# Kernel tuning notes

Measured on AMD Instinct MI355X. Metric: run time of the kernel, lower is better.

The kernel has to match this reference:

```python
import jax, jax.numpy as jnp
import numpy as np

B, N, C, H, D = 4, 2048, 1024, 16, 64
EPS = 1e-6

def setup_inputs() -> dict:
    key = jax.random.key(0)
    k1, k2, k3 = jax.random.split(key, 3)
    hidden_states = jax.random.normal(k1, (B, N, C), dtype=jnp.float32)
    qkv_w = jax.random.normal(k2, (3 * C, C), dtype=jnp.float32) * (C ** -0.5)
    out_w = jax.random.normal(k3, (C, C), dtype=jnp.float32) * (C ** -0.5)
    norm_q_w = jnp.ones((D,), dtype=jnp.float32)
    norm_k_w = jnp.ones((D,), dtype=jnp.float32)
    # RoPE tables: standard theta=10000 frequencies, rotate-half convention
    inv_freq = 1.0 / (10000.0 ** (jnp.arange(0, D, 2, dtype=jnp.float32) / D))
    pos = jnp.arange(N, dtype=jnp.float32)
    angles = pos[:, None] * inv_freq[None, :]              # [N, D/2]
    angles = jnp.concatenate([angles, angles], axis=-1)    # [N, D]
    cos = jnp.cos(angles)
    sin = jnp.sin(angles)
    return {"hidden_states": hidden_states, "cos": cos, "sin": sin,
            "qkv_w": qkv_w, "out_w": out_w,
            "norm_q_w": norm_q_w, "norm_k_w": norm_k_w}

def _rms_norm(x, w):
    # RMSNorm over last dim (head_dim)
    var = jnp.mean(jnp.square(x), axis=-1, keepdims=True)
    return x * jax.lax.rsqrt(var + EPS) * w

def _rotate_half(x):
    x1, x2 = jnp.split(x, 2, axis=-1)
    return jnp.concatenate([-x2, x1], axis=-1)

def reference(hidden_states, cos, sin, qkv_w, out_w, norm_q_w, norm_k_w):
    # fused QKV projection: [B,N,C] -> [B,N,3,H,D]
    qkv = jnp.einsum('bnc,oc->bno', hidden_states, qkv_w).reshape(B, N, 3, H, D)
    q, k, v = qkv[:, :, 0], qkv[:, :, 1], qkv[:, :, 2]   # each [B,N,H,D]
    q = _rms_norm(q, norm_q_w)
    k = _rms_norm(k, norm_k_w)
    # RoPE, broadcast cos/sin [N,D] -> [1,N,1,D]
    c = cos[None, :, None, :]
    s = sin[None, :, None, :]
    q = q * c + _rotate_half(q) * s
    k = k * c + _rotate_half(k) * s
    # SDPA: softmax(q k^T / sqrt(D)) v, no mask
    scale = D ** -0.5
    scores = jnp.einsum('bqhd,bkhd->bhqk', q, k) * scale   # [B,H,N,N]
    probs = jax.nn.softmax(scores, axis=-1)
    attn = jnp.einsum('bhqk,bkhd->bqhd', probs, v).reshape(B, N, C)
    return jnp.einsum('bnc,oc->bno', attn, out_w)
```

## Files before the change

### kernel.cpp

```cpp
#include <hip/hip_runtime.h>
#include <hip/hip_bf16.h>

typedef short bf16x8 __attribute__((ext_vector_type(8)));
typedef float f32x4 __attribute__((ext_vector_type(4)));
typedef float f32x16 __attribute__((ext_vector_type(16)));
typedef __hip_bfloat16 bf16;
typedef unsigned int uint;

static constexpr int Bn = 4, Nn = 2048, Cn = 1024, Hn = 16, Dn = 64;
static constexpr float kEps = 1e-6f;
static constexpr float kQScale = 0.125f * 1.44269504088896340f;

#define GLOAD_LDS16(gp, lp)                                                        \
  __builtin_amdgcn_global_load_lds(                                                \
      (const __attribute__((address_space(1))) unsigned int*)(gp),                 \
      (__attribute__((address_space(3))) unsigned int*)(lp), 16, 0, 0)

__device__ __forceinline__ float exp2_raw(float x) {
  float r;
  asm("v_exp_f32 %0, %1" : "=v"(r) : "v"(x));
  return r;
}

__global__ __launch_bounds__(256) void cvt_kernel(const float* __restrict__ in,
                                                  bf16* __restrict__ out, int n4) {
  int i = blockIdx.x * 256 + threadIdx.x;
  if (i >= n4) return;
  const float4 v = reinterpret_cast<const float4*>(in)[i];
  bf16 t[4];
  t[0] = __float2bfloat16(v.x); t[1] = __float2bfloat16(v.y);
  t[2] = __float2bfloat16(v.z); t[3] = __float2bfloat16(v.w);
  reinterpret_cast<uint2*>(out)[i] = *reinterpret_cast<const uint2*>(t);
}

template <int EPI>
__global__ __launch_bounds__(256) void gemm_bt(
    const bf16* __restrict__ A, const bf16* __restrict__ Bw,
    float* __restrict__ Cf, bf16* __restrict__ q_raw, bf16* __restrict__ k_raw,
    bf16* __restrict__ v_buf, const float* __restrict__ cosb,
    const float* __restrict__ sinb, const float* __restrict__ nqw,
    const float* __restrict__ nkw, int N, int K) {
  __shared__ __align__(16) bf16 As[128 * 64];
  __shared__ __align__(16) bf16 Bs[128 * 64];
  const int tid = threadIdx.x;
  const int lane = tid & 63, w = tid >> 6;
  const int wr = w >> 1, wc = w & 1;
  const int l15 = lane & 15, l4 = lane >> 4;
  const int m0 = blockIdx.y * 128, n0 = blockIdx.x * 128;
  f32x4 acc[4][4] = {};

  const int sr = tid >> 3, sc = (tid & 7) * 8;
  const bf16* const Ap = A + (size_t)(m0 + sr) * K + sc;
  const bf16* const Bp = Bw + (size_t)(n0 + sr) * K + sc;
  char* const asd = (char*)As + tid * 16;
  char* const bsd = (char*)Bs + tid * 16;

  for (int k0 = 0; k0 < K; k0 += 64) {
    __syncthreads();
#pragma unroll
    for (int c = 0; c < 4; ++c) {
      GLOAD_LDS16(Ap + (size_t)(c * 32) * K + k0, asd + c * 4096);
      GLOAD_LDS16(Bp + (size_t)(c * 32) * K + k0, bsd + c * 4096);
    }
    __syncthreads();
#pragma unroll
    for (int kc = 0; kc < 2; ++kc) {
      bf16x8 af[4], bfr[4];
#pragma unroll
      for (int mi = 0; mi < 4; ++mi)
        af[mi] = *reinterpret_cast<const bf16x8*>(
            (const char*)As + (wr * 64 + mi * 16 + l15) * 128 + kc * 64 + l4 * 16);
#pragma unroll
      for (int ni = 0; ni < 4; ++ni)
        bfr[ni] = *reinterpret_cast<const bf16x8*>(
            (const char*)Bs + (wc * 64 + ni * 16 + l15) * 128 + kc * 64 + l4 * 16);
#pragma unroll
      for (int mi = 0; mi < 4; ++mi)
#pragma unroll
        for (int ni = 0; ni < 4; ++ni)
          acc[mi][ni] =
              __builtin_amdgcn_mfma_f32_16x16x32_bf16(af[mi], bfr[ni], acc[mi][ni], 0, 0, 0);
    }
  }

  if (EPI == 1) {
#pragma unroll
    for (int mi = 0; mi < 4; ++mi)
#pragma unroll
      for (int ni = 0; ni < 4; ++ni)
#pragma unroll
        for (int r = 0; r < 4; ++r) {
          const int row = m0 + wr * 64 + mi * 16 + l4 * 4 + r;
          const int col = n0 + wc * 64 + ni * 16 + l15;
          Cf[(size_t)row * N + col] = acc[mi][ni][r];
        }
    return;
  }

  const int colbase = n0 + wc * 64;
  const int which = colbase >> 10;
  const int hh = (colbase >> 6) & 15;
  if (which == 2) {
#pragma unroll
    for (int mi = 0; mi < 4; ++mi)
#pragma unroll
      for (int r = 0; r < 4; ++r) {
        const int row = m0 + wr * 64 + mi * 16 + l4 * 4 + r;
        const int b = row >> 11, n = row & (Nn - 1);
#pragma unroll
        for (int ni = 0; ni < 4; ++ni) {
          const int d = ni * 16 + l15;
          const size_t idx = (((size_t)b * Hn + hh) * Nn + n) * Dn + d;
          v_buf[idx] = __float2bfloat16(acc[mi][ni][r]);
        }
      }
    return;
  }
  const float* const wgt = which ? nkw : nqw;
  bf16* const dst = which ? k_raw : q_raw;
  float wv4[4];
#pragma unroll
  for (int ni = 0; ni < 4; ++ni) wv4[ni] = wgt[ni * 16 + l15];
#pragma unroll
  for (int mi = 0; mi < 4; ++mi)
#pragma unroll
    for (int r = 0; r < 4; ++r) {
      const int row = m0 + wr * 64 + mi * 16 + l4 * 4 + r;
      const int b = row >> 11, n = row & (Nn - 1);
      float x0 = acc[mi][0][r], x1 = acc[mi][1][r], x2 = acc[mi][2][r], x3 = acc[mi][3][r];
      float ss = x0 * x0 + x1 * x1 + x2 * x2 + x3 * x3;
      ss += __shfl_xor(ss, 1);
      ss += __shfl_xor(ss, 2);
      ss += __shfl_xor(ss, 4);
      ss += __shfl_xor(ss, 8);
      const float rinv = rsqrtf(ss * (1.f / Dn) + kEps);
      float nx[4] = {x0 * rinv * wv4[0], x1 * rinv * wv4[1], x2 * rinv * wv4[2],
                     x3 * rinv * wv4[3]};
#pragma unroll
      for (int ni = 0; ni < 4; ++ni) {
        const int d = ni * 16 + l15;
        const float c = cosb[n * Dn + d], s = sinb[n * Dn + d];
        const float sgn = (ni < 2) ? -1.f : 1.f;
        float val = nx[ni] * c + sgn * nx[ni ^ 2] * s;
        if (which == 0) val *= kQScale;
        const size_t idx = (((size_t)b * Hn + hh) * Nn + n) * Dn + d;
        dst[idx] = __float2bfloat16(val);
      }
    }
}

__global__ __launch_bounds__(256, 3) void flash_attn(
    const bf16* __restrict__ Qb, const bf16* __restrict__ Kb,
    const bf16* __restrict__ Vb, bf16* __restrict__ Ob) {
  __shared__ __align__(16) char KsB[2][32 * 128];
  __shared__ __align__(16) char VtB[2][64 * 64];
  const int bh = blockIdx.y;
  const int q0 = blockIdx.x * 128;
  const int tid = threadIdx.x, lane = tid & 63, w = tid >> 6;
  const int l31 = lane & 31, hi = lane >> 5;
  const bf16* Qp = Qb + (size_t)bh * Nn * Dn;
  const bf16* Kp = Kb + (size_t)bh * Nn * Dn;
  const bf16* Vp = Vb + (size_t)bh * Nn * Dn;

  const int qrow = q0 + w * 32 + l31;
  bf16x8 qf[4];
#pragma unroll
  for (int dm = 0; dm < 4; ++dm)
    qf[dm] = *reinterpret_cast<const bf16x8*>(&Qp[(size_t)qrow * Dn + dm * 16 + hi * 8]);

  f32x16 Ot0 = {}, Ot1 = {};
  float m_r = -1e30f, l_r = 0.f;

  const int skk = tid >> 3, sd0 = (tid & 7) * 8;
  const int srcKe = (((sd0 * 2) ^ ((skk & 7) << 4)) >> 1);

  auto stage_v = [&](char* Vn, const uint4& a) {
    const uint wa[4] = {a.x, a.y, a.z, a.w};
#pragma unroll
    for (int j = 0; j < 8; ++j) {
      const int d = sd0 + j;
      const int xs = (((d >> 1) ^ (d >> 3)) & 3) << 4;
      const unsigned short va = (j & 1) ? (unsigned short)(wa[j >> 1] >> 16)
                                        : (unsigned short)(wa[j >> 1] & 0xffff);
      *reinterpret_cast<unsigned short*>(Vn + d * 64 + ((skk * 2) ^ xs)) = va;
    }
  };

  GLOAD_LDS16(Kp + (size_t)skk * Dn + srcKe, KsB[0] + tid * 16);
  {
    uint4 cv = *reinterpret_cast<const uint4*>(&Vp[(size_t)skk * Dn + sd0]);
    stage_v(VtB[0], cv);
  }
  uint4 nv = *reinterpret_cast<const uint4*>(&Vp[(size_t)(32 + skk) * Dn + sd0]);
  __syncthreads();

  const int swzk_rd = (l31 & 7) << 4;
  const int xs0 = ((((l31) >> 1) ^ ((l31) >> 3)) & 3) << 4;
  const int xs1 = ((((32 + l31) >> 1) ^ ((32 + l31) >> 3)) & 3) << 4;
  int cur = 0;
  for (int k0 = 0; k0 < Nn; k0 += 32) {
    const char* Kc = KsB[cur];
    const char* Vc = VtB[cur];

    if (k0 + 32 < Nn) {
      GLOAD_LDS16(Kp + (size_t)(k0 + 32 + skk) * Dn + srcKe, KsB[cur ^ 1] + tid * 16);
      stage_v(VtB[cur ^ 1], nv);
      if (k0 + 64 < Nn)
        nv = *reinterpret_cast<const uint4*>(&Vp[(size_t)(k0 + 64 + skk) * Dn + sd0]);
    }

    f32x16 S0 = {};
    __builtin_amdgcn_s_setprio(1);
#pragma unroll
    for (int dm = 0; dm < 4; ++dm) {
      bf16x8 kf = *reinterpret_cast<const bf16x8*>(
          Kc + l31 * 128 + ((dm * 32 + hi * 16) ^ swzk_rd));
      S0 = __builtin_amdgcn_mfma_f32_32x32x16_bf16(kf, qf[dm], S0, 0, 0, 0);
    }
    __builtin_amdgcn_s_setprio(0);

    float tm8[8];
#pragma unroll
    for (int i = 0; i < 8; ++i) tm8[i] = fmaxf(S0[i], S0[i + 8]);
#pragma unroll
    for (int i = 0; i < 4; ++i) tm8[i] = fmaxf(tm8[i], tm8[i + 4]);
    float mx = fmaxf(fmaxf(tm8[0], tm8[1]), fmaxf(tm8[2], tm8[3]));
    const float full = fmaxf(mx, __shfl_xor(mx, 32));
    if (__any(full > m_r + 8.f)) {
      const float mnew = fmaxf(m_r, full);
      const float al = exp2_raw(m_r - mnew);
#pragma unroll
      for (int i = 0; i < 16; ++i) { Ot0[i] *= al; Ot1[i] *= al; }
      l_r *= al;
      m_r = mnew;
    }
#pragma unroll
    for (int i = 0; i < 16; ++i) S0[i] = exp2_raw(S0[i] - m_r);
    float ps = 0.f;
    uint wv[8];
#pragma unroll
    for (int c = 0; c < 2; ++c) {
      ps += ((S0[8 * c + 0] + S0[8 * c + 1]) + (S0[8 * c + 2] + S0[8 * c + 3])) +
            ((S0[8 * c + 4] + S0[8 * c + 5]) + (S0[8 * c + 6] + S0[8 * c + 7]));
      uint w0, w1, w2, w3;
      asm("v_cvt_pk_bf16_f32 %0, %1, %2" : "=v"(w0) : "v"(S0[8 * c + 0]), "v"(S0[8 * c + 1]));
      asm("v_cvt_pk_bf16_f32 %0, %1, %2" : "=v"(w1) : "v"(S0[8 * c + 2]), "v"(S0[8 * c + 3]));
      asm("v_cvt_pk_bf16_f32 %0, %1, %2" : "=v"(w2) : "v"(S0[8 * c + 4]), "v"(S0[8 * c + 5]));
      asm("v_cvt_pk_bf16_f32 %0, %1, %2" : "=v"(w3) : "v"(S0[8 * c + 6]), "v"(S0[8 * c + 7]));
      asm("v_permlane32_swap_b32 %0, %1" : "+v"(w0), "+v"(w2));
      asm("v_permlane32_swap_b32 %0, %1" : "+v"(w1), "+v"(w3));
      wv[c * 4 + 0] = w0; wv[c * 4 + 1] = w1;
      wv[c * 4 + 2] = w2; wv[c * 4 + 3] = w3;
    }
    ps += __shfl_xor(ps, 32);
    l_r += ps;

    __builtin_amdgcn_s_setprio(1);
#pragma unroll
    for (int s = 0; s < 2; ++s) {
      const uint4 uu = {wv[s * 4 + 0], wv[s * 4 + 1], wv[s * 4 + 2], wv[s * 4 + 3]};
      const bf16x8 pa = __builtin_bit_cast(bf16x8, uu);
      bf16x8 vf0 = *reinterpret_cast<const bf16x8*>(
          Vc + l31 * 64 + ((s * 32 + hi * 16) ^ xs0));
      Ot0 = __builtin_amdgcn_mfma_f32_32x32x16_bf16(vf0, pa, Ot0, 0, 0, 0);
      bf16x8 vf1 = *reinterpret_cast<const bf16x8*>(
          Vc + (32 + l31) * 64 + ((s * 32 + hi * 16) ^ xs1));
      Ot1 = __builtin_amdgcn_mfma_f32_32x32x16_bf16(vf1, pa, Ot1, 0, 0, 0);
    }
    __builtin_amdgcn_s_setprio(0);

    __syncthreads();
    cur ^= 1;
  }

  const float inv = 1.f / l_r;
  const int b = bh >> 4, h = bh & 15;
#pragma unroll
  for (int dc = 0; dc < 2; ++dc)
#pragma unroll
    for (int a2 = 0; a2 < 4; ++a2) {
      const f32x16& O = dc ? Ot1 : Ot0;
      unsigned short u0 = __bfloat16_as_ushort(__float2bfloat16(O[a2 * 4 + 0] * inv));
      unsigned short u1 = __bfloat16_as_ushort(__float2bfloat16(O[a2 * 4 + 1] * inv));
      unsigned short u2 = __bfloat16_as_ushort(__float2bfloat16(O[a2 * 4 + 2] * inv));
      unsigned short u3 = __bfloat16_as_ushort(__float2bfloat16(O[a2 * 4 + 3] * inv));
      uint2 pk;
      pk.x = (uint)u0 | ((uint)u1 << 16);
      pk.y = (uint)u2 | ((uint)u3 << 16);
      const int col = h * 64 + dc * 32 + a2 * 8 + hi * 4;
      *reinterpret_cast<uint2*>(&Ob[((size_t)(b * Nn + qrow)) * Cn + col]) = pk;
    }
}

extern "C" void kernel_launch(void* const* d_in, const int* in_sizes, int n_in,
                              void* d_out, int out_size, void* d_ws, size_t ws_size,
                              hipStream_t stream) {
  const float* hs   = (const float*)d_in[0];
  const float* cosb = (const float*)d_in[1];
  const float* sinb = (const float*)d_in[2];
  const float* qkvw = (const float*)d_in[3];
  const float* outw = (const float*)d_in[4];
  const float* nqw  = (const float*)d_in[5];
  const float* nkw  = (const float*)d_in[6];
  float* out = (float*)d_out;

  char* ws = (char*)d_ws;
  size_t off = 0;
  bf16* hs_b   = (bf16*)(ws + off); off += (size_t)Bn * Nn * Cn * 2;
  bf16* qkvw_b = (bf16*)(ws + off); off += (size_t)3 * Cn * Cn * 2;
  bf16* outw_b = (bf16*)(ws + off); off += (size_t)Cn * Cn * 2;
  bf16* q_raw  = (bf16*)(ws + off); off += (size_t)Bn * Hn * Nn * Dn * 2;
  bf16* k_raw  = (bf16*)(ws + off); off += (size_t)Bn * Hn * Nn * Dn * 2;
  bf16* v_buf  = (bf16*)(ws + off); off += (size_t)Bn * Hn * Nn * Dn * 2;
  bf16* attn   = (bf16*)(ws + off); off += (size_t)Bn * Nn * Cn * 2;

  cvt_kernel<<<(Bn * Nn * Cn / 4 + 255) / 256, 256, 0, stream>>>(hs, hs_b, Bn * Nn * Cn / 4);
  cvt_kernel<<<(3 * Cn * Cn / 4 + 255) / 256, 256, 0, stream>>>(qkvw, qkvw_b, 3 * Cn * Cn / 4);
  cvt_kernel<<<(Cn * Cn / 4 + 255) / 256, 256, 0, stream>>>(outw, outw_b, Cn * Cn / 4);

  gemm_bt<0><<<dim3(3 * Cn / 128, Bn * Nn / 128), 256, 0, stream>>>(
      hs_b, qkvw_b, nullptr, q_raw, k_raw, v_buf, cosb, sinb, nqw, nkw, 3 * Cn, Cn);

  flash_attn<<<dim3(Nn / 128, Bn * Hn), 256, 0, stream>>>(q_raw, k_raw, v_buf, attn);

  gemm_bt<1><<<dim3(Cn / 128, Bn * Nn / 128), 256, 0, stream>>>(
      attn, outw_b, out, nullptr, nullptr, nullptr, nullptr, nullptr, nullptr, nullptr,
      Cn, Cn);
}
```

Before: 236.9 us.

## Remap GEMM tiles per XCD, raise flash-attn occupancy, linearize max reduction

The GEMMs now launch on a 1D grid and remap block ids so that each of the 8 XCDs gets a contiguous band of N-tiles and iterates over M. The aim is that blocks sharing weight tiles land on the same XCD's L2. The flash attention launch bound is raised from 3 to 4 waves per SIMD, which caps register use to allow more resident blocks at some risk of spills. The row-max reduction is rewritten as a sequential fmax chain, likely meant to fold into three-operand max instructions.

```diff
diff --git a/kernel.cpp b/kernel.cpp
--- a/kernel.cpp
+++ b/kernel.cpp
@@ -39,14 +39,19 @@
     float* __restrict__ Cf, bf16* __restrict__ q_raw, bf16* __restrict__ k_raw,
     bf16* __restrict__ v_buf, const float* __restrict__ cosb,
     const float* __restrict__ sinb, const float* __restrict__ nqw,
-    const float* __restrict__ nkw, int N, int K) {
+    const float* __restrict__ nkw, int nxt, int nyt, int N, int K) {
   __shared__ __align__(16) bf16 As[128 * 64];
   __shared__ __align__(16) bf16 Bs[128 * 64];
   const int tid = threadIdx.x;
   const int lane = tid & 63, w = tid >> 6;
   const int wr = w >> 1, wc = w & 1;
   const int l15 = lane & 15, l4 = lane >> 4;
-  const int m0 = blockIdx.y * 128, n0 = blockIdx.x * 128;
+  const int bid = blockIdx.x;
+  const int xcd = bid & 7;
+  const int kk2 = bid >> 3;
+  const int ntile = xcd * (nxt >> 3) + kk2 / nyt;
+  const int mtile = kk2 % nyt;
+  const int m0 = mtile * 128, n0 = ntile * 128;
   f32x4 acc[4][4] = {};
 
   const int sr = tid >> 3, sc = (tid & 7) * 8;
@@ -149,7 +154,7 @@
     }
 }
 
-__global__ __launch_bounds__(256, 3) void flash_attn(
+__global__ __launch_bounds__(256, 4) void flash_attn(
     const bf16* __restrict__ Qb, const bf16* __restrict__ Kb,
     const bf16* __restrict__ Vb, bf16* __restrict__ Ob) {
   __shared__ __align__(16) char KsB[2][32 * 128];
@@ -219,12 +224,14 @@
     }
     __builtin_amdgcn_s_setprio(0);
 
-    float tm8[8];
-#pragma unroll
-    for (int i = 0; i < 8; ++i) tm8[i] = fmaxf(S0[i], S0[i + 8]);
-#pragma unroll
-    for (int i = 0; i < 4; ++i) tm8[i] = fmaxf(tm8[i], tm8[i + 4]);
-    float mx = fmaxf(fmaxf(tm8[0], tm8[1]), fmaxf(tm8[2], tm8[3]));
+    float mx = fmaxf(fmaxf(S0[0], S0[1]), S0[2]);
+    mx = fmaxf(fmaxf(mx, S0[3]), S0[4]);
+    mx = fmaxf(fmaxf(mx, S0[5]), S0[6]);
+    mx = fmaxf(fmaxf(mx, S0[7]), S0[8]);
+    mx = fmaxf(fmaxf(mx, S0[9]), S0[10]);
+    mx = fmaxf(fmaxf(mx, S0[11]), S0[12]);
+    mx = fmaxf(fmaxf(mx, S0[13]), S0[14]);
+    mx = fmaxf(mx, S0[15]);
     const float full = fmaxf(mx, __shfl_xor(mx, 32));
     if (__any(full > m_r + 8.f)) {
       const float mnew = fmaxf(m_r, full);
@@ -318,12 +325,13 @@
   cvt_kernel<<<(3 * Cn * Cn / 4 + 255) / 256, 256, 0, stream>>>(qkvw, qkvw_b, 3 * Cn * Cn / 4);
   cvt_kernel<<<(Cn * Cn / 4 + 255) / 256, 256, 0, stream>>>(outw, outw_b, Cn * Cn / 4);
 
-  gemm_bt<0><<<dim3(3 * Cn / 128, Bn * Nn / 128), 256, 0, stream>>>(
-      hs_b, qkvw_b, nullptr, q_raw, k_raw, v_buf, cosb, sinb, nqw, nkw, 3 * Cn, Cn);
+  gemm_bt<0><<<24 * 64, 256, 0, stream>>>(
+      hs_b, qkvw_b, nullptr, q_raw, k_raw, v_buf, cosb, sinb, nqw, nkw,
+      24, 64, 3 * Cn, Cn);
 
   flash_attn<<<dim3(Nn / 128, Bn * Hn), 256, 0, stream>>>(q_raw, k_raw, v_buf, attn);
 
-  gemm_bt<1><<<dim3(Cn / 128, Bn * Nn / 128), 256, 0, stream>>>(
+  gemm_bt<1><<<8 * 64, 256, 0, stream>>>(
       attn, outw_b, out, nullptr, nullptr, nullptr, nullptr, nullptr, nullptr, nullptr,
-      Cn, Cn);
-}
+      8, 64, Cn, Cn);
+}
```

Measured after the change: 235.3 us. About the same (-0.7%).
